# Performance work log

Measured on AMD Instinct MI355X. Metric: run time of the kernel, lower is better.

## Reference

```python
import jax, jax.numpy as jnp
import numpy as np

NG, NC, FG, FC, D = 8192, 4096, 512, 256, 64
ALPHA = 0.2          # leaky_relu negative slope
NEG = -9.0e15        # mask fill value from the torch code


def _leaky(x):
    return jnp.where(x >= 0, x, ALPHA * x)


def _relation(h_src, h_dst, a, adj):
    # additive GAT score: e[i,j] = leaky(h_src[i]@a[:D] + h_dst[j]@a[D:])
    s1 = h_src @ a[:D]            # [Ns]
    s2 = h_dst @ a[D:]            # [Nd]
    e = _leaky(s1[:, None] + s2[None, :])          # [Ns, Nd]
    att = jax.nn.softmax(jnp.where(adj > 0, e, NEG), axis=1)
    return att @ h_dst            # [Ns, D]


def setup_inputs() -> dict:
    key = jax.random.key(0)
    ks = jax.random.split(key, 14)
    sc = 0.05
    return {
        "gene_x": jax.random.normal(ks[0], (NG, FG), jnp.float32),
        "cell_x": jax.random.normal(ks[1], (NC, FC), jnp.float32),
        "W_g": jax.random.normal(ks[2], (FG, D), jnp.float32) * sc,
        "W_c": jax.random.normal(ks[3], (FC, D), jnp.float32) * sc,
        "a_gg": jax.random.normal(ks[4], (2 * D,), jnp.float32) * sc,
        "a_gc": jax.random.normal(ks[5], (2 * D,), jnp.float32) * sc,
        "a_cc": jax.random.normal(ks[6], (2 * D,), jnp.float32) * sc,
        "a_cg": jax.random.normal(ks[7], (2 * D,), jnp.float32) * sc,
        "Wgate_g": jax.random.normal(ks[8], (D, 1), jnp.float32) * sc,
        "bgate_g": jnp.full((1,), -2.0, jnp.float32),
        "Wgate_c": jax.random.normal(ks[9], (D, 1), jnp.float32) * sc,
        "bgate_c": jnp.full((1,), -2.0, jnp.float32),
        "gene_adj": jax.random.randint(ks[10], (NG, NG), 0, 2, jnp.int32),
        "cell_adj": jax.random.randint(ks[11], (NC, NC), 0, 2, jnp.int32),
        "gene_cell_adj": jax.random.randint(ks[12], (NG, NC), 0, 2, jnp.int32),
    }


def reference(gene_x, cell_x, W_g, W_c, a_gg, a_gc, a_cc, a_cg,
              Wgate_g, bgate_g, Wgate_c, bgate_c,
              gene_adj, cell_adj, gene_cell_adj):
    gene_h = gene_x @ W_g                              # [NG, D]
    cell_h = cell_x @ W_c                              # [NC, D]

    gene_from_gene = _relation(gene_h, gene_h, a_gg, gene_adj)
    gene_from_cell = _relation(gene_h, cell_h, a_gc, gene_cell_adj)
    cell_from_cell = _relation(cell_h, cell_h, a_cc, cell_adj)
    cell_from_gene = _relation(cell_h, gene_h, a_cg, gene_cell_adj.T)

    gamma_g = jax.nn.sigmoid(gene_h @ Wgate_g + bgate_g)   # [NG, 1]
    gamma_c = jax.nn.sigmoid(cell_h @ Wgate_c + bgate_c)   # [NC, 1]

    gene_out = _leaky(gene_h + gene_from_gene + gamma_g * gene_from_cell)
    cell_out = _leaky(cell_h + cell_from_cell + gamma_c * cell_from_gene)
    return gene_out, cell_out
```

## Files before the change

### kernel.cpp

```cpp
#include <hip/hip_runtime.h>

#define NG 8192
#define NC 4096
#define FG 512
#define FC 256
#define ALPHA 0.2f

typedef float f32x4 __attribute__((ext_vector_type(4)));
typedef short bf16x8 __attribute__((ext_vector_type(8)));

static __device__ __forceinline__ float leakyf(float x) { return fmaxf(x, ALPHA * x); }

static __device__ __forceinline__ unsigned short f2bf(float f) {
    unsigned u = __builtin_bit_cast(unsigned, f);
    u += 0x7fffu + ((u >> 16) & 1u);
    return (unsigned short)(u >> 16);
}

static __device__ __forceinline__ unsigned pack2bf(float lo, float hi) {
    return __builtin_amdgcn_perm(__builtin_bit_cast(unsigned, hi),
                                 __builtin_bit_cast(unsigned, lo), 0x07060302u);
}

static __device__ __forceinline__ float wred(float v) {
#pragma unroll
    for (int m = 1; m < 64; m <<= 1) v += __shfl_xor(v, m, 64);
    return v;
}

#define PACK_BLKS ((NG + NC + NG) / 4)
#define PROJ_BLKS (NG / 16 + NC / 16)

static __device__ __forceinline__ void proj_body(
    const float* __restrict__ x, const float* __restrict__ W, int K, int N,
    float* __restrict__ h, unsigned short* __restrict__ hT,
    const float* __restrict__ aA, const float* __restrict__ aB,
    const float* __restrict__ aC, const float* __restrict__ aD,
    const float* __restrict__ aG, const float* __restrict__ bG,
    float* __restrict__ sA, float* __restrict__ sB, float* __restrict__ sC,
    float* __restrict__ sD, float* __restrict__ gam, int blk)
{
    const int wave = threadIdx.x >> 6, lane = threadIdx.x & 63;
    const int r0 = blk * 16 + wave * 4;
    const float* xr = x + (size_t)r0 * K;
    float acc0 = 0.f, acc1 = 0.f, acc2 = 0.f, acc3 = 0.f;
    for (int k = 0; k < K; k += 4) {
        float4 x0 = *(const float4*)(xr + k);
        float4 x1 = *(const float4*)(xr + K + k);
        float4 x2 = *(const float4*)(xr + 2 * (size_t)K + k);
        float4 x3 = *(const float4*)(xr + 3 * (size_t)K + k);
        float w0 = W[(k + 0) * 64 + lane];
        float w1 = W[(k + 1) * 64 + lane];
        float w2 = W[(k + 2) * 64 + lane];
        float w3 = W[(k + 3) * 64 + lane];
        acc0 += x0.x * w0 + x0.y * w1 + x0.z * w2 + x0.w * w3;
        acc1 += x1.x * w0 + x1.y * w1 + x1.z * w2 + x1.w * w3;
        acc2 += x2.x * w0 + x2.y * w1 + x2.z * w2 + x2.w * w3;
        acc3 += x3.x * w0 + x3.y * w1 + x3.z * w2 + x3.w * w3;
    }
    float accs[4] = {acc0, acc1, acc2, acc3};
    unsigned short hb[4];
#pragma unroll
    for (int t = 0; t < 4; t++) {
        h[(size_t)(r0 + t) * 64 + lane] = accs[t];
        hb[t] = f2bf(accs[t]);
    }
    *(ushort4*)&hT[(size_t)lane * N + r0] = make_ushort4(hb[0], hb[1], hb[2], hb[3]);

    const float cA = aA[lane], cB = aB[lane], cC = aC[lane], cD = aD[lane], cG = aG[lane];
    const float bias = bG[0];
#pragma unroll
    for (int t = 0; t < 4; t++) {
        float vA = wred(accs[t] * cA);
        float vB = wred(accs[t] * cB);
        float vC = wred(accs[t] * cC);
        float vD = wred(accs[t] * cD);
        float vG = wred(accs[t] * cG);
        if (lane == 0) {
            sA[r0 + t] = vA; sB[r0 + t] = vB; sC[r0 + t] = vC; sD[r0 + t] = vD;
            gam[r0 + t] = 1.f / (1.f + __expf(-(vG + bias)));
        }
    }
}

__global__ __launch_bounds__(256) void prep_all(
    const int* __restrict__ gene_adj, const int* __restrict__ cell_adj,
    const int* __restrict__ gc_adj,
    unsigned char* __restrict__ bmGG, unsigned char* __restrict__ bmCC,
    unsigned char* __restrict__ bmGC,
    const float* __restrict__ gene_x, const float* __restrict__ W_g,
    const float* __restrict__ cell_x, const float* __restrict__ W_c,
    float* __restrict__ gene_h, unsigned short* __restrict__ gene_hT,
    float* __restrict__ cell_h, unsigned short* __restrict__ cell_hT,
    const float* __restrict__ a_gg, const float* __restrict__ a_gc,
    const float* __restrict__ a_cc, const float* __restrict__ a_cg,
    const float* __restrict__ Wgg, const float* __restrict__ bgg,
    const float* __restrict__ Wgc, const float* __restrict__ bgc,
    float* s1gg, float* s2gg, float* s1gc, float* s2cg, float* gamg,
    float* s1cc, float* s2cc, float* s2gc, float* s1cg, float* gamc)
{
    if (blockIdx.x < PACK_BLKS) {
        const int wave = threadIdx.x >> 6, lane = threadIdx.x & 63;
        const int r = blockIdx.x * 4 + wave;
        const int* row; unsigned char* brow; int C;
        if (r < NG)           { row = gene_adj + (size_t)r * NG;              brow = bmGG + (size_t)r * (NG >> 3);              C = NG; }
        else if (r < NG + NC) { int rr = r - NG;      row = cell_adj + (size_t)rr * NC; brow = bmCC + (size_t)rr * (NC >> 3); C = NC; }
        else                  { int rr = r - NG - NC; row = gc_adj   + (size_t)rr * NC; brow = bmGC + (size_t)rr * (NC >> 3); C = NC; }
        for (int j = lane * 8; j < C; j += 512) {
            int4 a0 = *(const int4*)(row + j);
            int4 a1 = *(const int4*)(row + j + 4);
            unsigned b = (unsigned)(a0.x > 0)        | ((unsigned)(a0.y > 0) << 1)
                       | ((unsigned)(a0.z > 0) << 2) | ((unsigned)(a0.w > 0) << 3)
                       | ((unsigned)(a1.x > 0) << 4) | ((unsigned)(a1.y > 0) << 5)
                       | ((unsigned)(a1.z > 0) << 6) | ((unsigned)(a1.w > 0) << 7);
            brow[j >> 3] = (unsigned char)b;
        }
    } else {
        int blk = blockIdx.x - PACK_BLKS;
        if (blk < NG / 16)
            proj_body(gene_x, W_g, FG, NG, gene_h, gene_hT,
                      a_gg, a_gg + 64, a_gc, a_cg + 64, Wgg, bgg,
                      s1gg, s2gg, s1gc, s2cg, gamg, blk);
        else
            proj_body(cell_x, W_c, FC, NC, cell_h, cell_hT,
                      a_cc, a_cc + 64, a_gc + 64, a_cg, Wgc, bgc,
                      s1cc, s2cc, s2gc, s1cg, gamc, blk - NG / 16);
    }
}

static __device__ __forceinline__ void rel_chunk_compute(
    const unsigned short* hbuf, const float* s2buf,
    unsigned mask_words[8], float s1v, int m, int kp,
    f32x4& acc0, f32x4& acc1, f32x4& acc2, f32x4& acc3, f32x4& acc4,
    const bf16x8 bones)
{
#pragma unroll
    for (int g = 0; g < 8; ++g) {
        const int jl = g * 32 + kp * 8;
        float4 sa = *(const float4*)&s2buf[jl];
        float4 sb = *(const float4*)&s2buf[jl + 4];
        unsigned byte = (mask_words[g] >> (kp * 8)) & 0xffu;
        bf16x8 b0 = *(const bf16x8*)&hbuf[(0 * 16 + m) * 264 + jl];
        bf16x8 b1 = *(const bf16x8*)&hbuf[(1 * 16 + m) * 264 + jl];
        bf16x8 b2 = *(const bf16x8*)&hbuf[(2 * 16 + m) * 264 + jl];
        bf16x8 b3 = *(const bf16x8*)&hbuf[(3 * 16 + m) * 264 + jl];
        float s2v[8] = {sa.x, sa.y, sa.z, sa.w, sb.x, sb.y, sb.z, sb.w};
        float w[8];
#pragma unroll
        for (int t = 0; t < 8; t++) {
            float e = s1v + s2v[t];
            w[t] = ((byte >> t) & 1u) ? __expf(leakyf(e)) : 0.f;
        }
        uint4 pk = {pack2bf(w[0], w[1]), pack2bf(w[2], w[3]),
                    pack2bf(w[4], w[5]), pack2bf(w[6], w[7])};
        bf16x8 af = __builtin_bit_cast(bf16x8, pk);
        acc0 = __builtin_amdgcn_mfma_f32_16x16x32_bf16(af, b0, acc0, 0, 0, 0);
        acc1 = __builtin_amdgcn_mfma_f32_16x16x32_bf16(af, b1, acc1, 0, 0, 0);
        acc2 = __builtin_amdgcn_mfma_f32_16x16x32_bf16(af, b2, acc2, 0, 0, 0);
        acc3 = __builtin_amdgcn_mfma_f32_16x16x32_bf16(af, b3, acc3, 0, 0, 0);
        acc4 = __builtin_amdgcn_mfma_f32_16x16x32_bf16(af, bones, acc4, 0, 0, 0);
    }
}

static __device__ __forceinline__ void rel_epilogue(
    const f32x4& acc0, const f32x4& acc1, const f32x4& acc2, const f32x4& acc3,
    const f32x4& acc4, float* __restrict__ num, float* __restrict__ lsum,
    int Ns, int p, int strip, int wave, int m, int kp)
{
    const int orow0 = strip * 64 + wave * 16 + kp * 4;
#pragma unroll
    for (int r = 0; r < 4; r++) {
        size_t base = ((size_t)p * Ns + orow0 + r) * 64;
        num[base + m]      = acc0[r];
        num[base + 16 + m] = acc1[r];
        num[base + 32 + m] = acc2[r];
        num[base + 48 + m] = acc3[r];
        if (m == 0) lsum[(size_t)p * Ns + orow0 + r] = acc4[r];
    }
}

static __device__ __forceinline__ void rel_row_body(
    unsigned short* hbuf, float* s2buf,
    const unsigned char* __restrict__ bm, int bm_ld,
    const float* __restrict__ s1, const float* __restrict__ s2,
    const unsigned short* __restrict__ hT, int Nd,
    float* __restrict__ num, float* __restrict__ lsum, int Ns, int JS,
    int strip, int p)
{
    const int wave = threadIdx.x >> 6, lane = threadIdx.x & 63;
    const int m = lane & 15, kp = lane >> 4;
    const int jlen = Nd / JS, jbase = p * jlen;
    const int i_row = strip * 64 + wave * 16 + m;
    const float s1v = s1[i_row];
    const unsigned char* bmrow = bm + (size_t)i_row * bm_ld;
    bf16x8 bones;
#pragma unroll
    for (int t = 0; t < 8; t++) bones[t] = (short)0x3f80;
    f32x4 acc0 = {0.f, 0.f, 0.f, 0.f}, acc1 = acc0, acc2 = acc0, acc3 = acc0, acc4 = acc0;

    for (int jc = jbase; jc < jbase + jlen; jc += 256) {
        uint4 q0 = *(const uint4*)(bmrow + (jc >> 3));
        uint4 q1 = *(const uint4*)(bmrow + (jc >> 3) + 16);
        for (int idx = threadIdx.x; idx < 2048; idx += 256) {
            int c = idx >> 5, off = (idx & 31) * 8;
            *(int4*)&hbuf[c * 264 + off] = *(const int4*)&hT[(size_t)c * Nd + jc + off];
        }
        s2buf[threadIdx.x] = s2[jc + threadIdx.x];
        __syncthreads();
        unsigned words[8] = {q0.x, q0.y, q0.z, q0.w, q1.x, q1.y, q1.z, q1.w};
        rel_chunk_compute(hbuf, s2buf, words, s1v, m, kp, acc0, acc1, acc2, acc3, acc4, bones);
        __syncthreads();
    }
    rel_epilogue(acc0, acc1, acc2, acc3, acc4, num, lsum, Ns, p, strip, wave, m, kp);
}

static __device__ __forceinline__ void rel_col_body(
    unsigned short* hbuf, float* s2buf,
    const unsigned char* __restrict__ bm, int bm_ld,
    const float* __restrict__ s1, const float* __restrict__ s2,
    const unsigned short* __restrict__ hT, int Nd,
    float* __restrict__ num, float* __restrict__ lsum, int Ns, int JS,
    int strip, int p)
{
    const int wave = threadIdx.x >> 6, lane = threadIdx.x & 63;
    const int m = lane & 15, kp = lane >> 4;
    const int jlen = Nd / JS, jbase = p * jlen;
    const int i_row = strip * 64 + wave * 16 + m;
    const float s1v = s1[i_row];
    const int bcol = i_row >> 3, bbit = i_row & 7;
    bf16x8 bones;
#pragma unroll
    for (int t = 0; t < 8; t++) bones[t] = (short)0x3f80;
    f32x4 acc0 = {0.f, 0.f, 0.f, 0.f}, acc1 = acc0, acc2 = acc0, acc3 = acc0, acc4 = acc0;

    for (int jc = jbase; jc < jbase + jlen; jc += 256) {
        for (int idx = threadIdx.x; idx < 2048; idx += 256) {
            int c = idx >> 5, off = (idx & 31) * 8;
            *(int4*)&hbuf[c * 264 + off] = *(const int4*)&hT[(size_t)c * Nd + jc + off];
        }
        s2buf[threadIdx.x] = s2[jc + threadIdx.x];
        __syncthreads();
#pragma unroll
        for (int g = 0; g < 8; ++g) {
            const int jl = g * 32 + kp * 8;
            const int jg = jc + jl;
            const unsigned char* bp = bm + (size_t)jg * bm_ld + bcol;
            unsigned mw = 0;
#pragma unroll
            for (int t = 0; t < 8; t++)
                mw |= ((unsigned)((bp[(size_t)t * bm_ld] >> bbit) & 1u)) << t;
            float4 sa = *(const float4*)&s2buf[jl];
            float4 sb = *(const float4*)&s2buf[jl + 4];
            bf16x8 b0 = *(const bf16x8*)&hbuf[(0 * 16 + m) * 264 + jl];
            bf16x8 b1 = *(const bf16x8*)&hbuf[(1 * 16 + m) * 264 + jl];
            bf16x8 b2 = *(const bf16x8*)&hbuf[(2 * 16 + m) * 264 + jl];
            bf16x8 b3 = *(const bf16x8*)&hbuf[(3 * 16 + m) * 264 + jl];
            float s2v[8] = {sa.x, sa.y, sa.z, sa.w, sb.x, sb.y, sb.z, sb.w};
            float w[8];
#pragma unroll
            for (int t = 0; t < 8; t++) {
                float e = s1v + s2v[t];
                w[t] = ((mw >> t) & 1u) ? __expf(leakyf(e)) : 0.f;
            }
            uint4 pk = {pack2bf(w[0], w[1]), pack2bf(w[2], w[3]),
                        pack2bf(w[4], w[5]), pack2bf(w[6], w[7])};
            bf16x8 af = __builtin_bit_cast(bf16x8, pk);
            acc0 = __builtin_amdgcn_mfma_f32_16x16x32_bf16(af, b0, acc0, 0, 0, 0);
            acc1 = __builtin_amdgcn_mfma_f32_16x16x32_bf16(af, b1, acc1, 0, 0, 0);
            acc2 = __builtin_amdgcn_mfma_f32_16x16x32_bf16(af, b2, acc2, 0, 0, 0);
            acc3 = __builtin_amdgcn_mfma_f32_16x16x32_bf16(af, b3, acc3, 0, 0, 0);
            acc4 = __builtin_amdgcn_mfma_f32_16x16x32_bf16(af, bones, acc4, 0, 0, 0);
        }
        __syncthreads();
    }
    rel_epilogue(acc0, acc1, acc2, acc3, acc4, num, lsum, Ns, p, strip, wave, m, kp);
}

__global__ __launch_bounds__(256, 4) void rel_fused(
    const unsigned char* __restrict__ bmGG, const unsigned char* __restrict__ bmCC,
    const unsigned char* __restrict__ bmGC,
    const float* __restrict__ s1gg, const float* __restrict__ s2gg,
    const float* __restrict__ s1cc, const float* __restrict__ s2cc,
    const float* __restrict__ s1gc, const float* __restrict__ s2gc,
    const float* __restrict__ s1cg, const float* __restrict__ s2cg,
    const unsigned short* __restrict__ gene_hT, const unsigned short* __restrict__ cell_hT,
    float* __restrict__ numGG, float* __restrict__ lGG,
    float* __restrict__ numCC, float* __restrict__ lCC,
    float* __restrict__ numGC, float* __restrict__ lGC,
    float* __restrict__ numCG, float* __restrict__ lCG)
{
    __shared__ __align__(16) unsigned short hbuf[64 * 264];
    __shared__ __align__(16) float s2buf[256];
    const int b = blockIdx.x;
    if (b < 1024) {
        const int w = b;
        rel_row_body(hbuf, s2buf, bmGG, NG / 8, s1gg, s2gg, gene_hT, NG,
                     numGG, lGG, NG, 8, w >> 3, w & 7);
    } else if (b < 1536) {
        const int w = b - 1024;
        rel_row_body(hbuf, s2buf, bmCC, NC / 8, s1cc, s2cc, cell_hT, NC,
                     numCC, lCC, NC, 8, w >> 3, w & 7);
    } else if (b < 2048) {
        const int w = b - 1536;
        rel_row_body(hbuf, s2buf, bmGC, NC / 8, s1gc, s2gc, cell_hT, NC,
                     numGC, lGC, NG, 4, w >> 2, w & 3);
    } else {
        const int w = b - 2048;
        rel_col_body(hbuf, s2buf, bmGC, NC / 8, s1cg, s2cg, gene_hT, NG,
                     numCG, lCG, NC, 8, w >> 3, w & 7);
    }
}

static __device__ __forceinline__ void combine_body(
    const float* __restrict__ numS, const float* __restrict__ lS, int JSS,
    const float* __restrict__ numX, const float* __restrict__ lX, int JSX,
    int Ns, const float* __restrict__ h, const float* __restrict__ gam,
    float* __restrict__ out, int blk)
{
    int idx = blk * 256 + threadIdx.x;
    int i = idx >> 6, c = idx & 63;
    float nS = 0.f, dS = 0.f, nX = 0.f, dX = 0.f;
    for (int p = 0; p < JSS; p++) {
        nS += numS[((size_t)p * Ns + i) * 64 + c];
        dS += lS[(size_t)p * Ns + i];
    }
    for (int p = 0; p < JSX; p++) {
        nX += numX[((size_t)p * Ns + i) * 64 + c];
        dX += lX[(size_t)p * Ns + i];
    }
    float v = h[idx] + nS / dS + gam[i] * (nX / dX);
    out[idx] = leakyf(v);
}

__global__ __launch_bounds__(256) void combine_all(
    const float* __restrict__ numGG, const float* __restrict__ lGG,
    const float* __restrict__ numGC, const float* __restrict__ lGC,
    const float* __restrict__ numCC, const float* __restrict__ lCC,
    const float* __restrict__ numCG, const float* __restrict__ lCG,
    const float* __restrict__ gene_h, const float* __restrict__ cell_h,
    const float* __restrict__ gamg, const float* __restrict__ gamc,
    float* __restrict__ out_gene, float* __restrict__ out_cell)
{
    if (blockIdx.x < NG * 64 / 256)
        combine_body(numGG, lGG, 8, numGC, lGC, 4, NG, gene_h, gamg, out_gene, blockIdx.x);
    else
        combine_body(numCC, lCC, 8, numCG, lCG, 8, NC, cell_h, gamc, out_cell,
                     blockIdx.x - NG * 64 / 256);
}

extern "C" void kernel_launch(void* const* d_in, const int* in_sizes, int n_in,
                              void* d_out, int out_size, void* d_ws, size_t ws_size,
                              hipStream_t stream)
{
    const float* gene_x = (const float*)d_in[0];
    const float* cell_x = (const float*)d_in[1];
    const float* W_g    = (const float*)d_in[2];
    const float* W_c    = (const float*)d_in[3];
    const float* a_gg   = (const float*)d_in[4];
    const float* a_gc   = (const float*)d_in[5];
    const float* a_cc   = (const float*)d_in[6];
    const float* a_cg   = (const float*)d_in[7];
    const float* Wgg    = (const float*)d_in[8];
    const float* bgg    = (const float*)d_in[9];
    const float* Wgc    = (const float*)d_in[10];
    const float* bgc    = (const float*)d_in[11];
    const int* gene_adj = (const int*)d_in[12];
    const int* cell_adj = (const int*)d_in[13];
    const int* gc_adj   = (const int*)d_in[14];

    size_t off = 0;
    char* wsb = (char*)d_ws;
    auto alloc = [&](size_t bytes) -> void* {
        void* p = wsb + off;
        off += (bytes + 255) & ~(size_t)255;
        return p;
    };
    const int JS_GG = 8, JS_CC = 8, JS_GC = 4, JS_CG = 8;

    float* gene_h = (float*)alloc((size_t)NG * 64 * 4);
    float* cell_h = (float*)alloc((size_t)NC * 64 * 4);
    unsigned short* gene_hT = (unsigned short*)alloc((size_t)NG * 64 * 2);
    unsigned short* cell_hT = (unsigned short*)alloc((size_t)NC * 64 * 2);
    unsigned char* bmGG = (unsigned char*)alloc((size_t)NG * (NG / 8));
    unsigned char* bmCC = (unsigned char*)alloc((size_t)NC * (NC / 8));
    unsigned char* bmGC = (unsigned char*)alloc((size_t)NG * (NC / 8));
    float* s1gg = (float*)alloc(NG * 4);
    float* s2gg = (float*)alloc(NG * 4);
    float* s1gc = (float*)alloc(NG * 4);
    float* s2cg = (float*)alloc(NG * 4);
    float* gamg = (float*)alloc(NG * 4);
    float* s1cc = (float*)alloc(NC * 4);
    float* s2cc = (float*)alloc(NC * 4);
    float* s2gc = (float*)alloc(NC * 4);
    float* s1cg = (float*)alloc(NC * 4);
    float* gamc = (float*)alloc(NC * 4);
    float* numGG = (float*)alloc((size_t)NG * 64 * JS_GG * 4);
    float* lGG   = (float*)alloc((size_t)NG * JS_GG * 4);
    float* numGC = (float*)alloc((size_t)NG * 64 * JS_GC * 4);
    float* lGC   = (float*)alloc((size_t)NG * JS_GC * 4);
    float* numCC = (float*)alloc((size_t)NC * 64 * JS_CC * 4);
    float* lCC   = (float*)alloc((size_t)NC * JS_CC * 4);
    float* numCG = (float*)alloc((size_t)NC * 64 * JS_CG * 4);
    float* lCG   = (float*)alloc((size_t)NC * JS_CG * 4);

    float* out_gene = (float*)d_out;
    float* out_cell = (float*)d_out + (size_t)NG * 64;

    prep_all<<<PACK_BLKS + PROJ_BLKS, 256, 0, stream>>>(
        gene_adj, cell_adj, gc_adj, bmGG, bmCC, bmGC,
        gene_x, W_g, cell_x, W_c, gene_h, gene_hT, cell_h, cell_hT,
        a_gg, a_gc, a_cc, a_cg, Wgg, bgg, Wgc, bgc,
        s1gg, s2gg, s1gc, s2cg, gamg, s1cc, s2cc, s2gc, s1cg, gamc);

    rel_fused<<<2560, 256, 0, stream>>>(bmGG, bmCC, bmGC,
        s1gg, s2gg, s1cc, s2cc, s1gc, s2gc, s1cg, s2cg,
        gene_hT, cell_hT,
        numGG, lGG, numCC, lCC, numGC, lGC, numCG, lCG);

    combine_all<<<(NG + NC) * 64 / 256, 256, 0, stream>>>(
        numGG, lGG, numGC, lGC, numCC, lCC, numCG, lCG,
        gene_h, cell_h, gamg, gamc, out_gene, out_cell);
}
```

Before: 645.9 us.

## Halve relation chunk width to 128 columns and raise occupancy to 6 blocks

Shrinks the shared-memory tile in the fused relation kernel from 256 to 128 destination columns per chunk (LDS row stride 136), and raises the launch-bounds minimum blocks per CU from 4 to 6 so more blocks can be resident. It also splits the combined prep kernel into separate adjacency-packing and projection kernels and reorders the packing rows so the gene-cell adjacency is handled first. The goal is better latency hiding from higher occupancy. The cost is twice as many barrier and load iterations per block, a tighter register budget, and one extra kernel launch.

```diff
diff --git a/kernel.cpp b/kernel.cpp
--- a/kernel.cpp
+++ b/kernel.cpp
@@ -28,8 +28,28 @@
     return v;
 }
 
-#define PACK_BLKS ((NG + NC + NG) / 4)
-#define PROJ_BLKS (NG / 16 + NC / 16)
+__global__ __launch_bounds__(256) void pack_all(
+    const int* __restrict__ gene_adj, const int* __restrict__ cell_adj,
+    const int* __restrict__ gc_adj,
+    unsigned char* __restrict__ bmGG, unsigned char* __restrict__ bmCC,
+    unsigned char* __restrict__ bmGC)
+{
+    const int wave = threadIdx.x >> 6, lane = threadIdx.x & 63;
+    const int r = blockIdx.x * 4 + wave;
+    const int* row; unsigned char* brow; int C;
+    if (r < NG)           { row = gc_adj   + (size_t)r * NC;              brow = bmGC + (size_t)r * (NC >> 3);              C = NC; }
+    else if (r < NG + NC) { int rr = r - NG;      row = cell_adj + (size_t)rr * NC; brow = bmCC + (size_t)rr * (NC >> 3); C = NC; }
+    else                  { int rr = r - NG - NC; row = gene_adj + (size_t)rr * NG; brow = bmGG + (size_t)rr * (NG >> 3); C = NG; }
+    for (int j = lane * 8; j < C; j += 512) {
+        int4 a0 = *(const int4*)(row + j);
+        int4 a1 = *(const int4*)(row + j + 4);
+        unsigned b = (unsigned)(a0.x > 0)        | ((unsigned)(a0.y > 0) << 1)
+                   | ((unsigned)(a0.z > 0) << 2) | ((unsigned)(a0.w > 0) << 3)
+                   | ((unsigned)(a1.x > 0) << 4) | ((unsigned)(a1.y > 0) << 5)
+                   | ((unsigned)(a1.z > 0) << 6) | ((unsigned)(a1.w > 0) << 7);
+        brow[j >> 3] = (unsigned char)b;
+    }
+}
 
 static __device__ __forceinline__ void proj_body(
     const float* __restrict__ x, const float* __restrict__ W, int K, int N,
@@ -83,11 +103,7 @@
     }
 }
 
-__global__ __launch_bounds__(256) void prep_all(
-    const int* __restrict__ gene_adj, const int* __restrict__ cell_adj,
-    const int* __restrict__ gc_adj,
-    unsigned char* __restrict__ bmGG, unsigned char* __restrict__ bmCC,
-    unsigned char* __restrict__ bmGC,
+__global__ __launch_bounds__(256) void proj_all(
     const float* __restrict__ gene_x, const float* __restrict__ W_g,
     const float* __restrict__ cell_x, const float* __restrict__ W_c,
     float* __restrict__ gene_h, unsigned short* __restrict__ gene_hT,
@@ -99,67 +115,14 @@
     float* s1gg, float* s2gg, float* s1gc, float* s2cg, float* gamg,
     float* s1cc, float* s2cc, float* s2gc, float* s1cg, float* gamc)
 {
-    if (blockIdx.x < PACK_BLKS) {
-        const int wave = threadIdx.x >> 6, lane = threadIdx.x & 63;
-        const int r = blockIdx.x * 4 + wave;
-        const int* row; unsigned char* brow; int C;
-        if (r < NG)           { row = gene_adj + (size_t)r * NG;              brow = bmGG + (size_t)r * (NG >> 3);              C = NG; }
-        else if (r < NG + NC) { int rr = r - NG;      row = cell_adj + (size_t)rr * NC; brow = bmCC + (size_t)rr * (NC >> 3); C = NC; }
-        else                  { int rr = r - NG - NC; row = gc_adj   + (size_t)rr * NC; brow = bmGC + (size_t)rr * (NC >> 3); C = NC; }
-        for (int j = lane * 8; j < C; j += 512) {
-            int4 a0 = *(const int4*)(row + j);
-            int4 a1 = *(const int4*)(row + j + 4);
-            unsigned b = (unsigned)(a0.x > 0)        | ((unsigned)(a0.y > 0) << 1)
-                       | ((unsigned)(a0.z > 0) << 2) | ((unsigned)(a0.w > 0) << 3)
-                       | ((unsigned)(a1.x > 0) << 4) | ((unsigned)(a1.y > 0) << 5)
-                       | ((unsigned)(a1.z > 0) << 6) | ((unsigned)(a1.w > 0) << 7);
-            brow[j >> 3] = (unsigned char)b;
-        }
-    } else {
-        int blk = blockIdx.x - PACK_BLKS;
-        if (blk < NG / 16)
-            proj_body(gene_x, W_g, FG, NG, gene_h, gene_hT,
-                      a_gg, a_gg + 64, a_gc, a_cg + 64, Wgg, bgg,
-                      s1gg, s2gg, s1gc, s2cg, gamg, blk);
-        else
-            proj_body(cell_x, W_c, FC, NC, cell_h, cell_hT,
-                      a_cc, a_cc + 64, a_gc + 64, a_cg, Wgc, bgc,
-                      s1cc, s2cc, s2gc, s1cg, gamc, blk - NG / 16);
-    }
-}
-
-static __device__ __forceinline__ void rel_chunk_compute(
-    const unsigned short* hbuf, const float* s2buf,
-    unsigned mask_words[8], float s1v, int m, int kp,
-    f32x4& acc0, f32x4& acc1, f32x4& acc2, f32x4& acc3, f32x4& acc4,
-    const bf16x8 bones)
-{
-#pragma unroll
-    for (int g = 0; g < 8; ++g) {
-        const int jl = g * 32 + kp * 8;
-        float4 sa = *(const float4*)&s2buf[jl];
-        float4 sb = *(const float4*)&s2buf[jl + 4];
-        unsigned byte = (mask_words[g] >> (kp * 8)) & 0xffu;
-        bf16x8 b0 = *(const bf16x8*)&hbuf[(0 * 16 + m) * 264 + jl];
-        bf16x8 b1 = *(const bf16x8*)&hbuf[(1 * 16 + m) * 264 + jl];
-        bf16x8 b2 = *(const bf16x8*)&hbuf[(2 * 16 + m) * 264 + jl];
-        bf16x8 b3 = *(const bf16x8*)&hbuf[(3 * 16 + m) * 264 + jl];
-        float s2v[8] = {sa.x, sa.y, sa.z, sa.w, sb.x, sb.y, sb.z, sb.w};
-        float w[8];
-#pragma unroll
-        for (int t = 0; t < 8; t++) {
-            float e = s1v + s2v[t];
-            w[t] = ((byte >> t) & 1u) ? __expf(leakyf(e)) : 0.f;
-        }
-        uint4 pk = {pack2bf(w[0], w[1]), pack2bf(w[2], w[3]),
-                    pack2bf(w[4], w[5]), pack2bf(w[6], w[7])};
-        bf16x8 af = __builtin_bit_cast(bf16x8, pk);
-        acc0 = __builtin_amdgcn_mfma_f32_16x16x32_bf16(af, b0, acc0, 0, 0, 0);
-        acc1 = __builtin_amdgcn_mfma_f32_16x16x32_bf16(af, b1, acc1, 0, 0, 0);
-        acc2 = __builtin_amdgcn_mfma_f32_16x16x32_bf16(af, b2, acc2, 0, 0, 0);
-        acc3 = __builtin_amdgcn_mfma_f32_16x16x32_bf16(af, b3, acc3, 0, 0, 0);
-        acc4 = __builtin_amdgcn_mfma_f32_16x16x32_bf16(af, bones, acc4, 0, 0, 0);
-    }
+    if (blockIdx.x < NG / 16)
+        proj_body(gene_x, W_g, FG, NG, gene_h, gene_hT,
+                  a_gg, a_gg + 64, a_gc, a_cg + 64, Wgg, bgg,
+                  s1gg, s2gg, s1gc, s2cg, gamg, blockIdx.x);
+    else
+        proj_body(cell_x, W_c, FC, NC, cell_h, cell_hT,
+                  a_cc, a_cc + 64, a_gc + 64, a_cg, Wgc, bgc,
+                  s1cc, s2cc, s2gc, s1cg, gamc, blockIdx.x - NG / 16);
 }
 
 static __device__ __forceinline__ void rel_epilogue(
@@ -198,17 +161,41 @@
     for (int t = 0; t < 8; t++) bones[t] = (short)0x3f80;
     f32x4 acc0 = {0.f, 0.f, 0.f, 0.f}, acc1 = acc0, acc2 = acc0, acc3 = acc0, acc4 = acc0;
 
-    for (int jc = jbase; jc < jbase + jlen; jc += 256) {
-        uint4 q0 = *(const uint4*)(bmrow + (jc >> 3));
-        uint4 q1 = *(const uint4*)(bmrow + (jc >> 3) + 16);
-        for (int idx = threadIdx.x; idx < 2048; idx += 256) {
-            int c = idx >> 5, off = (idx & 31) * 8;
-            *(int4*)&hbuf[c * 264 + off] = *(const int4*)&hT[(size_t)c * Nd + jc + off];
+    for (int jc = jbase; jc < jbase + jlen; jc += 128) {
+        uint4 q = *(const uint4*)(bmrow + (jc >> 3));
+        for (int idx = threadIdx.x; idx < 1024; idx += 256) {
+            int c = idx >> 4, off = (idx & 15) * 8;
+            *(int4*)&hbuf[c * 136 + off] = *(const int4*)&hT[(size_t)c * Nd + jc + off];
         }
-        s2buf[threadIdx.x] = s2[jc + threadIdx.x];
+        if (threadIdx.x < 128) s2buf[threadIdx.x] = s2[jc + threadIdx.x];
         __syncthreads();
-        unsigned words[8] = {q0.x, q0.y, q0.z, q0.w, q1.x, q1.y, q1.z, q1.w};
-        rel_chunk_compute(hbuf, s2buf, words, s1v, m, kp, acc0, acc1, acc2, acc3, acc4, bones);
+        unsigned words[4] = {q.x, q.y, q.z, q.w};
+#pragma unroll
+        for (int g = 0; g < 4; ++g) {
+            const int jl = g * 32 + kp * 8;
+            float4 sa = *(const float4*)&s2buf[jl];
+            float4 sb = *(const float4*)&s2buf[jl + 4];
+            unsigned byte = (words[g] >> (kp * 8)) & 0xffu;
+            bf16x8 b0 = *(const bf16x8*)&hbuf[(0 * 16 + m) * 136 + jl];
+            bf16x8 b1 = *(const bf16x8*)&hbuf[(1 * 16 + m) * 136 + jl];
+            bf16x8 b2 = *(const bf16x8*)&hbuf[(2 * 16 + m) * 136 + jl];
+            bf16x8 b3 = *(const bf16x8*)&hbuf[(3 * 16 + m) * 136 + jl];
+            float s2v[8] = {sa.x, sa.y, sa.z, sa.w, sb.x, sb.y, sb.z, sb.w};
+            float w[8];
+#pragma unroll
+            for (int t = 0; t < 8; t++) {
+                float e = s1v + s2v[t];
+                w[t] = ((byte >> t) & 1u) ? __expf(leakyf(e)) : 0.f;
+            }
+            uint4 pk = {pack2bf(w[0], w[1]), pack2bf(w[2], w[3]),
+                        pack2bf(w[4], w[5]), pack2bf(w[6], w[7])};
+            bf16x8 af = __builtin_bit_cast(bf16x8, pk);
+            acc0 = __builtin_amdgcn_mfma_f32_16x16x32_bf16(af, b0, acc0, 0, 0, 0);
+            acc1 = __builtin_amdgcn_mfma_f32_16x16x32_bf16(af, b1, acc1, 0, 0, 0);
+            acc2 = __builtin_amdgcn_mfma_f32_16x16x32_bf16(af, b2, acc2, 0, 0, 0);
+            acc3 = __builtin_amdgcn_mfma_f32_16x16x32_bf16(af, b3, acc3, 0, 0, 0);
+            acc4 = __builtin_amdgcn_mfma_f32_16x16x32_bf16(af, bones, acc4, 0, 0, 0);
+        }
         __syncthreads();
     }
     rel_epilogue(acc0, acc1, acc2, acc3, acc4, num, lsum, Ns, p, strip, wave, m, kp);
@@ -233,15 +220,15 @@
     for (int t = 0; t < 8; t++) bones[t] = (short)0x3f80;
     f32x4 acc0 = {0.f, 0.f, 0.f, 0.f}, acc1 = acc0, acc2 = acc0, acc3 = acc0, acc4 = acc0;
 
-    for (int jc = jbase; jc < jbase + jlen; jc += 256) {
-        for (int idx = threadIdx.x; idx < 2048; idx += 256) {
-            int c = idx >> 5, off = (idx & 31) * 8;
-            *(int4*)&hbuf[c * 264 + off] = *(const int4*)&hT[(size_t)c * Nd + jc + off];
+    for (int jc = jbase; jc < jbase + jlen; jc += 128) {
+        for (int idx = threadIdx.x; idx < 1024; idx += 256) {
+            int c = idx >> 4, off = (idx & 15) * 8;
+            *(int4*)&hbuf[c * 136 + off] = *(const int4*)&hT[(size_t)c * Nd + jc + off];
         }
-        s2buf[threadIdx.x] = s2[jc + threadIdx.x];
+        if (threadIdx.x < 128) s2buf[threadIdx.x] = s2[jc + threadIdx.x];
         __syncthreads();
 #pragma unroll
-        for (int g = 0; g < 8; ++g) {
+        for (int g = 0; g < 4; ++g) {
             const int jl = g * 32 + kp * 8;
             const int jg = jc + jl;
             const unsigned char* bp = bm + (size_t)jg * bm_ld + bcol;
@@ -251,10 +238,10 @@
                 mw |= ((unsigned)((bp[(size_t)t * bm_ld] >> bbit) & 1u)) << t;
             float4 sa = *(const float4*)&s2buf[jl];
             float4 sb = *(const float4*)&s2buf[jl + 4];
-            bf16x8 b0 = *(const bf16x8*)&hbuf[(0 * 16 + m) * 264 + jl];
-            bf16x8 b1 = *(const bf16x8*)&hbuf[(1 * 16 + m) * 264 + jl];
-            bf16x8 b2 = *(const bf16x8*)&hbuf[(2 * 16 + m) * 264 + jl];
-            bf16x8 b3 = *(const bf16x8*)&hbuf[(3 * 16 + m) * 264 + jl];
+            bf16x8 b0 = *(const bf16x8*)&hbuf[(0 * 16 + m) * 136 + jl];
+            bf16x8 b1 = *(const bf16x8*)&hbuf[(1 * 16 + m) * 136 + jl];
+            bf16x8 b2 = *(const bf16x8*)&hbuf[(2 * 16 + m) * 136 + jl];
+            bf16x8 b3 = *(const bf16x8*)&hbuf[(3 * 16 + m) * 136 + jl];
             float s2v[8] = {sa.x, sa.y, sa.z, sa.w, sb.x, sb.y, sb.z, sb.w};
             float w[8];
 #pragma unroll
@@ -276,7 +263,7 @@
     rel_epilogue(acc0, acc1, acc2, acc3, acc4, num, lsum, Ns, p, strip, wave, m, kp);
 }
 
-__global__ __launch_bounds__(256, 4) void rel_fused(
+__global__ __launch_bounds__(256, 6) void rel_fused(
     const unsigned char* __restrict__ bmGG, const unsigned char* __restrict__ bmCC,
     const unsigned char* __restrict__ bmGC,
     const float* __restrict__ s1gg, const float* __restrict__ s2gg,
@@ -289,8 +276,8 @@
     float* __restrict__ numGC, float* __restrict__ lGC,
     float* __restrict__ numCG, float* __restrict__ lCG)
 {
-    __shared__ __align__(16) unsigned short hbuf[64 * 264];
-    __shared__ __align__(16) float s2buf[256];
+    __shared__ __align__(16) unsigned short hbuf[64 * 136];
+    __shared__ __align__(16) float s2buf[128];
     const int b = blockIdx.x;
     if (b < 1024) {
         const int w = b;
@@ -406,8 +393,10 @@
     float* out_gene = (float*)d_out;
     float* out_cell = (float*)d_out + (size_t)NG * 64;
 
-    prep_all<<<PACK_BLKS + PROJ_BLKS, 256, 0, stream>>>(
-        gene_adj, cell_adj, gc_adj, bmGG, bmCC, bmGC,
+    pack_all<<<(NG + NC + NG) / 4, 256, 0, stream>>>(gene_adj, cell_adj, gc_adj,
+        bmGG, bmCC, bmGC);
+
+    proj_all<<<NG / 16 + NC / 16, 256, 0, stream>>>(
         gene_x, W_g, cell_x, W_c, gene_h, gene_hT, cell_h, cell_hT,
         a_gg, a_gc, a_cc, a_cg, Wgg, bgg, Wgc, bgc,
         s1gg, s2gg, s1gc, s2cg, gamg, s1cc, s2cc, s2gc, s1cg, gamc);
```

After: 635.3 us, median of 2. Within noise of the previous version (-1.6%).
